# Performance work log

Hardware: AMD Instinct MI355X
Metric: run time of the kernel (lower is better)

The kernel has to match this reference:

```python
import jax, jax.numpy as jnp
import numpy as np

ALPHA = 0.2  # LeakyReLU negative slope
N, IN_DIM, OUT_DIM = 8192, 128, 64


def setup_inputs() -> dict:
    key = jax.random.key(0)
    k1, k2, k3, k4 = jax.random.split(key, 4)
    x = jax.random.normal(k1, (N, IN_DIM), dtype=jnp.float32)
    adj = jax.random.randint(k2, (N, N), 0, 2, dtype=jnp.int32)
    W = jax.random.normal(k3, (IN_DIM, OUT_DIM), dtype=jnp.float32) * 0.1
    a = jax.random.normal(k4, (2 * OUT_DIM, 1), dtype=jnp.float32) * 0.1
    return {"x": x, "adj": adj, "W": W, "a": a}


def reference(x, adj, W, a):
    # h = x @ W : [N, out]
    h = x @ W
    # e_ij = LeakyReLU(a^T [h_i || h_j]) computed as broadcast sum of the
    # two halves of the attention vector (avoids materializing [N,N,2*out]).
    a_src = a[:OUT_DIM, 0]   # [out]
    a_dst = a[OUT_DIM:, 0]   # [out]
    e = (h @ a_src)[:, None] + (h @ a_dst)[None, :]      # [N, N]
    e = jnp.where(e > 0, e, ALPHA * e)                    # LeakyReLU
    # mask non-edges, row-softmax
    e = jnp.where(adj > 0, e, jnp.float32(-9e15))
    attn = jax.nn.softmax(e, axis=-1)                     # [N, N]
    out = attn @ h                                        # [N, out]
    # concat=True -> ELU nonlinearity
    return jax.nn.elu(out)
```

## Files before the change

kernel.cpp:

```cpp
#include <hip/hip_runtime.h>
#include <hip/hip_bf16.h>
#include <cstdint>
#include <cstddef>

#define N_NODES 8192
#define IN_DIM  128
#define OUT_DIM 64
#define LRELU_ALPHA 0.2f
#define LOG2E 1.44269504f
#define NSTEP 32

using f32x16 = __attribute__((ext_vector_type(16))) float;
using bf16x8 = __attribute__((ext_vector_type(8))) short;

typedef const __attribute__((address_space(1))) int* gas_ptr;
typedef __attribute__((address_space(3))) int* las_ptr;

static __device__ __forceinline__ unsigned short f2bf(float x) {
    union { float f; unsigned u; } v; v.f = x;
    unsigned r = v.u + 0x7FFFu + ((v.u >> 16) & 1u);
    return (unsigned short)(r >> 16);
}

__global__ __launch_bounds__(256) void gat_prep(
    const float* __restrict__ x, const float* __restrict__ W,
    const float* __restrict__ a,
    float* __restrict__ svec, float* __restrict__ dvec,
    unsigned short* __restrict__ hpack)
{
    __shared__ float shA[4][8][64];
    const int tid = threadIdx.x;
    const int w   = tid >> 6;
    const int f   = tid & 63;
    const int i0  = blockIdx.x * 8;

    float acc[8];
#pragma unroll
    for (int r = 0; r < 8; ++r) acc[r] = 0.f;

    const int k0 = w * 32;
#pragma unroll 2
    for (int k = k0; k < k0 + 32; k += 4) {
        const float w0 = W[(k + 0) * OUT_DIM + f];
        const float w1 = W[(k + 1) * OUT_DIM + f];
        const float w2 = W[(k + 2) * OUT_DIM + f];
        const float w3 = W[(k + 3) * OUT_DIM + f];
#pragma unroll
        for (int r = 0; r < 8; ++r) {
            const float4 xv = *reinterpret_cast<const float4*>(
                x + (size_t)(i0 + r) * IN_DIM + k);
            acc[r] = fmaf(xv.x, w0, acc[r]);
            acc[r] = fmaf(xv.y, w1, acc[r]);
            acc[r] = fmaf(xv.z, w2, acc[r]);
            acc[r] = fmaf(xv.w, w3, acc[r]);
        }
    }
#pragma unroll
    for (int r = 0; r < 8; ++r) shA[w][r][f] = acc[r];
    __syncthreads();

    if (w == 0) {
        union { unsigned short us[8]; int4 v; } pk;
#pragma unroll
        for (int r = 0; r < 8; ++r) {
            const float hv = shA[0][r][f] + shA[1][r][f] + shA[2][r][f] + shA[3][r][f];
            pk.us[r] = f2bf(hv);
        }
        const int jb    = i0 >> 4;
        const int jhalf = (i0 >> 3) & 1;
        const int fb    = f >> 5;
        const int lidx  = (f & 31) + 32 * jhalf;
        *reinterpret_cast<int4*>(hpack + ((size_t)(jb * 2 + fb) * 64 + lidx) * 8) = pk.v;
    } else if (w == 1) {
        const float asrc = a[f];
#pragma unroll
        for (int r = 0; r < 8; ++r) {
            const float hv = shA[0][r][f] + shA[1][r][f] + shA[2][r][f] + shA[3][r][f];
            float sv = hv * asrc;
#pragma unroll
            for (int off = 32; off >= 1; off >>= 1) sv += __shfl_xor(sv, off);
            if (f == 0) svec[i0 + r] = sv * LOG2E;
        }
    } else if (w == 2) {
        const float adst = a[OUT_DIM + f];
#pragma unroll
        for (int r = 0; r < 8; ++r) {
            const float hv = shA[0][r][f] + shA[1][r][f] + shA[2][r][f] + shA[3][r][f];
            float dv = hv * adst;
#pragma unroll
            for (int off = 32; off >= 1; off >>= 1) dv += __shfl_xor(dv, off);
            if (f == 0) dvec[i0 + r] = dv * LOG2E;
        }
    }
}

__global__ __launch_bounds__(512, 2) void gat_main(
    const int* __restrict__ adj,
    const float* __restrict__ svec, const float* __restrict__ dvec,
    const unsigned short* __restrict__ hpack,
    float* __restrict__ out)
{
    union SH {
        int tiles[2][32 * 256];
        struct { float red[8][32][64]; float redden[8][32]; } r;
    };
    __shared__ SH sh;

    const int tid = threadIdx.x;
    const int w   = tid >> 6;
    const int l   = tid & 63;
    const int rb  = blockIdx.x;
    const int row = l & 31;
    const int kh  = l >> 5;
    const int i0  = rb * 32;

    const float s_i = svec[i0 + row];
    asm volatile("" :: "v"(s_i));
    const bf16x8* hp = reinterpret_cast<const bf16x8*>(hpack);

    auto stage = [&](int buf, int ss) {
        const int jt0 = ss * 256;
#pragma unroll
        for (int q = 0; q < 4; ++q) {
            const int r0 = w * 4 + q;
            const int cg = l ^ (r0 & 7);
            const int* gsrc = adj + (size_t)(i0 + r0) * N_NODES + jt0 + cg * 4;
            int* ldst = &sh.tiles[buf][r0 * 256];
            __builtin_amdgcn_global_load_lds((gas_ptr)gsrc, (las_ptr)ldst, 16, 0, 0);
        }
    };

    f32x16 acc0, acc1;
#pragma unroll
    for (int r = 0; r < 16; ++r) { acc0[r] = 0.f; acc1[r] = 0.f; }
    float den = 0.f;

    stage(0, 0);
    stage(1, 1);

    const int swz = row & 7;
    for (int s = 0; s < NSTEP; ++s) {
        const int buf = s & 1;
        const int jg  = s * 256 + w * 32;
        const int jb  = jg >> 4;

        const bf16x8 b00 = hp[(jb * 2 + 0) * 64 + l];
        const bf16x8 b01 = hp[(jb * 2 + 1) * 64 + l];
        const bf16x8 b10 = hp[(jb * 2 + 2) * 64 + l];
        const bf16x8 b11 = hp[(jb * 2 + 3) * 64 + l];
        const int j0 = jg + kh * 8;
        const float4 dA0 = *reinterpret_cast<const float4*>(dvec + j0);
        const float4 dA1 = *reinterpret_cast<const float4*>(dvec + j0 + 4);
        const float4 dB0 = *reinterpret_cast<const float4*>(dvec + j0 + 16);
        const float4 dB1 = *reinterpret_cast<const float4*>(dvec + j0 + 20);

        if (s == NSTEP - 1) asm volatile("s_waitcnt vmcnt(8)"  ::: "memory");
        else                asm volatile("s_waitcnt vmcnt(12)" ::: "memory");
        __builtin_amdgcn_s_barrier();

        const int* tb = &sh.tiles[buf][0];
        const int c00 = w * 8 + kh * 2;
        const int c10 = w * 8 + 4 + kh * 2;
        const int4 A00 = *reinterpret_cast<const int4*>(&tb[row * 256 + ((c00    ) ^ swz) * 4]);
        const int4 A01 = *reinterpret_cast<const int4*>(&tb[row * 256 + ((c00 + 1) ^ swz) * 4]);
        const int4 A10 = *reinterpret_cast<const int4*>(&tb[row * 256 + ((c10    ) ^ swz) * 4]);
        const int4 A11 = *reinterpret_cast<const int4*>(&tb[row * 256 + ((c10 + 1) ^ swz) * 4]);
        asm volatile("s_waitcnt lgkmcnt(0)" ::: "memory");
        __builtin_amdgcn_s_barrier();

        if (s + 2 < NSTEP) stage(buf, s + 2);

        const float dd0[8] = {dA0.x, dA0.y, dA0.z, dA0.w, dA1.x, dA1.y, dA1.z, dA1.w};
        const int   ia0[8] = {A00.x, A00.y, A00.z, A00.w, A01.x, A01.y, A01.z, A01.w};
        const float dd1[8] = {dB0.x, dB0.y, dB0.z, dB0.w, dB1.x, dB1.y, dB1.z, dB1.w};
        const int   ia1[8] = {A10.x, A10.y, A10.z, A10.w, A11.x, A11.y, A11.z, A11.w};

        bf16x8 af0, af1;
#pragma unroll
        for (int e = 0; e < 8; ++e) {
            float ev = s_i + dd0[e];
            ev = fmaxf(ev, LRELU_ALPHA * ev);
            float pv = __builtin_amdgcn_exp2f(ev);
            pv = (ia0[e] > 0) ? pv : 0.f;
            union { float f; unsigned u; } pu; pu.f = pv;
            pu.u &= 0xFFFF0000u;
            den += pu.f;
            af0[e] = (short)(pu.u >> 16);
        }
#pragma unroll
        for (int e = 0; e < 8; ++e) {
            float ev = s_i + dd1[e];
            ev = fmaxf(ev, LRELU_ALPHA * ev);
            float pv = __builtin_amdgcn_exp2f(ev);
            pv = (ia1[e] > 0) ? pv : 0.f;
            union { float f; unsigned u; } pu; pu.f = pv;
            pu.u &= 0xFFFF0000u;
            den += pu.f;
            af1[e] = (short)(pu.u >> 16);
        }
        acc0 = __builtin_amdgcn_mfma_f32_32x32x16_bf16(af0, b00, acc0, 0, 0, 0);
        acc1 = __builtin_amdgcn_mfma_f32_32x32x16_bf16(af0, b01, acc1, 0, 0, 0);
        acc0 = __builtin_amdgcn_mfma_f32_32x32x16_bf16(af1, b10, acc0, 0, 0, 0);
        acc1 = __builtin_amdgcn_mfma_f32_32x32x16_bf16(af1, b11, acc1, 0, 0, 0);
    }

    __syncthreads();

#pragma unroll
    for (int r = 0; r < 16; ++r) {
        const int orow = (r & 3) + 8 * (r >> 2) + 4 * kh;
        sh.r.red[w][orow][row]      = acc0[r];
        sh.r.red[w][orow][32 + row] = acc1[r];
    }
    const float dtot = den + __shfl_xor(den, 32);
    if (l < 32) sh.r.redden[w][l] = dtot;
    __syncthreads();

    for (int e = tid; e < 32 * 64; e += 512) {
        const int orow = e >> 6;
        float v = 0.f, dsum = 0.f;
#pragma unroll
        for (int ww = 0; ww < 8; ++ww) {
            v    += sh.r.red[ww][orow][e & 63];
            dsum += sh.r.redden[ww][orow];
        }
        const float o = v / dsum;
        out[(size_t)(i0 + orow) * OUT_DIM + (e & 63)] = (o > 0.f) ? o : expm1f(o);
    }
}

extern "C" void kernel_launch(void* const* d_in, const int* in_sizes, int n_in,
                              void* d_out, int out_size, void* d_ws, size_t ws_size,
                              hipStream_t stream)
{
    const float* x   = (const float*)d_in[0];
    const int*   adj = (const int*)d_in[1];
    const float* W   = (const float*)d_in[2];
    const float* a   = (const float*)d_in[3];
    float* out = (float*)d_out;

    float* svec = (float*)d_ws;
    float* dvec = svec + N_NODES;
    unsigned short* hpack = (unsigned short*)(dvec + N_NODES);

    gat_prep<<<N_NODES / 8, 256, 0, stream>>>(x, W, a, svec, dvec, hpack);
    gat_main<<<256, 512, 0, stream>>>(adj, svec, dvec, hpack, out);
}
```

Before: 73.47 us.

## Warp-specialize: producer warps bit-pack adjacency, consumer warps run softmax-MFMA

Splits the 8 waves into 4 producer waves that load adjacency rows with plain global loads and compress them into 64-bit ballot masks in LDS, and 4 consumer waves that read the bitmasks and do the exp/mask/MFMA work. Granules of 2048 columns are double-buffered so compression of the next granule overlaps compute on the current one. This replaces the direct global-to-LDS int tile staging and shrinks the LDS footprint, but halves the number of waves doing the compute and MFMA work.

Result: slower. 83.43 us (+13.6%).

```diff
diff --git a/kernel.cpp b/kernel.cpp
--- a/kernel.cpp
+++ b/kernel.cpp
@@ -8,13 +8,11 @@
 #define OUT_DIM 64
 #define LRELU_ALPHA 0.2f
 #define LOG2E 1.44269504f
-#define NSTEP 32
+#define NG 4
 
 using f32x16 = __attribute__((ext_vector_type(16))) float;
 using bf16x8 = __attribute__((ext_vector_type(8))) short;
-
-typedef const __attribute__((address_space(1))) int* gas_ptr;
-typedef __attribute__((address_space(3))) int* las_ptr;
+typedef unsigned long long u64;
 
 static __device__ __forceinline__ unsigned short f2bf(float x) {
     union { float f; unsigned u; } v; v.f = x;
@@ -101,8 +99,8 @@
     float* __restrict__ out)
 {
     union SH {
-        int tiles[2][32 * 256];
-        struct { float red[8][32][64]; float redden[8][32]; } r;
+        u64 bits[2][32][32];
+        struct { float red[4][32][64]; float redden[4][32]; } r;
     };
     __shared__ SH sh;
 
@@ -114,19 +112,37 @@
     const int kh  = l >> 5;
     const int i0  = rb * 32;
 
-    const float s_i = svec[i0 + row];
-    asm volatile("" :: "v"(s_i));
     const bf16x8* hp = reinterpret_cast<const bf16x8*>(hpack);
-
-    auto stage = [&](int buf, int ss) {
-        const int jt0 = ss * 256;
-#pragma unroll
-        for (int q = 0; q < 4; ++q) {
-            const int r0 = w * 4 + q;
-            const int cg = l ^ (r0 & 7);
-            const int* gsrc = adj + (size_t)(i0 + r0) * N_NODES + jt0 + cg * 4;
-            int* ldst = &sh.tiles[buf][r0 * 256];
-            __builtin_amdgcn_global_load_lds((gas_ptr)gsrc, (las_ptr)ldst, 16, 0, 0);
+    const float s_i = (w >= 4) ? svec[i0 + row] : 0.f;
+
+    auto loadRow = [&](int (&av)[32], int r32, int j0) {
+        const int* base = adj + (size_t)(i0 + r32) * N_NODES + j0;
+#pragma unroll
+        for (int q = 0; q < 32; ++q) av[q] = base[q * 64 + l];
+    };
+    auto packRow = [&](const int (&av)[32], int r32, int buf) {
+        unsigned lo = 0, hi = 0;
+#pragma unroll
+        for (int q = 0; q < 32; ++q) {
+            const u64 b = __ballot(av[q] != 0);
+            if (l == q) { lo = (unsigned)b; hi = (unsigned)(b >> 32); }
+        }
+        if (l < 32) sh.bits[buf][r32][l ^ (r32 & 15)] = ((u64)hi << 32) | lo;
+    };
+    auto compressGranule = [&](int g, int buf) {
+        const int j0 = g * 2048;
+        int avA[32], avB[32];
+        loadRow(avA, w * 8, j0);
+#pragma unroll
+        for (int r8 = 0; r8 < 8; ++r8) {
+            const int r32 = w * 8 + r8;
+            if (r8 & 1) {
+                if (r8 + 1 < 8) loadRow(avA, r32 + 1, j0);
+                packRow(avB, r32, buf);
+            } else {
+                if (r8 + 1 < 8) loadRow(avB, r32 + 1, j0);
+                packRow(avA, r32, buf);
+            }
         }
     };
 
@@ -135,92 +151,96 @@
     for (int r = 0; r < 16; ++r) { acc0[r] = 0.f; acc1[r] = 0.f; }
     float den = 0.f;
 
-    stage(0, 0);
-    stage(1, 1);
-
-    const int swz = row & 7;
-    for (int s = 0; s < NSTEP; ++s) {
-        const int buf = s & 1;
-        const int jg  = s * 256 + w * 32;
-        const int jb  = jg >> 4;
-
-        const bf16x8 b00 = hp[(jb * 2 + 0) * 64 + l];
-        const bf16x8 b01 = hp[(jb * 2 + 1) * 64 + l];
-        const bf16x8 b10 = hp[(jb * 2 + 2) * 64 + l];
-        const bf16x8 b11 = hp[(jb * 2 + 3) * 64 + l];
-        const int j0 = jg + kh * 8;
-        const float4 dA0 = *reinterpret_cast<const float4*>(dvec + j0);
-        const float4 dA1 = *reinterpret_cast<const float4*>(dvec + j0 + 4);
-        const float4 dB0 = *reinterpret_cast<const float4*>(dvec + j0 + 16);
-        const float4 dB1 = *reinterpret_cast<const float4*>(dvec + j0 + 20);
-
-        if (s == NSTEP - 1) asm volatile("s_waitcnt vmcnt(8)"  ::: "memory");
-        else                asm volatile("s_waitcnt vmcnt(12)" ::: "memory");
-        __builtin_amdgcn_s_barrier();
-
-        const int* tb = &sh.tiles[buf][0];
-        const int c00 = w * 8 + kh * 2;
-        const int c10 = w * 8 + 4 + kh * 2;
-        const int4 A00 = *reinterpret_cast<const int4*>(&tb[row * 256 + ((c00    ) ^ swz) * 4]);
-        const int4 A01 = *reinterpret_cast<const int4*>(&tb[row * 256 + ((c00 + 1) ^ swz) * 4]);
-        const int4 A10 = *reinterpret_cast<const int4*>(&tb[row * 256 + ((c10    ) ^ swz) * 4]);
-        const int4 A11 = *reinterpret_cast<const int4*>(&tb[row * 256 + ((c10 + 1) ^ swz) * 4]);
-        asm volatile("s_waitcnt lgkmcnt(0)" ::: "memory");
-        __builtin_amdgcn_s_barrier();
-
-        if (s + 2 < NSTEP) stage(buf, s + 2);
-
-        const float dd0[8] = {dA0.x, dA0.y, dA0.z, dA0.w, dA1.x, dA1.y, dA1.z, dA1.w};
-        const int   ia0[8] = {A00.x, A00.y, A00.z, A00.w, A01.x, A01.y, A01.z, A01.w};
-        const float dd1[8] = {dB0.x, dB0.y, dB0.z, dB0.w, dB1.x, dB1.y, dB1.z, dB1.w};
-        const int   ia1[8] = {A10.x, A10.y, A10.z, A10.w, A11.x, A11.y, A11.z, A11.w};
-
-        bf16x8 af0, af1;
-#pragma unroll
-        for (int e = 0; e < 8; ++e) {
-            float ev = s_i + dd0[e];
-            ev = fmaxf(ev, LRELU_ALPHA * ev);
-            float pv = __builtin_amdgcn_exp2f(ev);
-            pv = (ia0[e] > 0) ? pv : 0.f;
-            union { float f; unsigned u; } pu; pu.f = pv;
-            pu.u &= 0xFFFF0000u;
-            den += pu.f;
-            af0[e] = (short)(pu.u >> 16);
-        }
-#pragma unroll
-        for (int e = 0; e < 8; ++e) {
-            float ev = s_i + dd1[e];
-            ev = fmaxf(ev, LRELU_ALPHA * ev);
-            float pv = __builtin_amdgcn_exp2f(ev);
-            pv = (ia1[e] > 0) ? pv : 0.f;
-            union { float f; unsigned u; } pu; pu.f = pv;
-            pu.u &= 0xFFFF0000u;
-            den += pu.f;
-            af1[e] = (short)(pu.u >> 16);
-        }
-        acc0 = __builtin_amdgcn_mfma_f32_32x32x16_bf16(af0, b00, acc0, 0, 0, 0);
-        acc1 = __builtin_amdgcn_mfma_f32_32x32x16_bf16(af0, b01, acc1, 0, 0, 0);
-        acc0 = __builtin_amdgcn_mfma_f32_32x32x16_bf16(af1, b10, acc0, 0, 0, 0);
-        acc1 = __builtin_amdgcn_mfma_f32_32x32x16_bf16(af1, b11, acc1, 0, 0, 0);
-    }
-
+    auto computeGranule = [&](int g, int buf) {
+        const int cw = w - 4;
+#pragma unroll
+        for (int c = 0; c < 8; ++c) {
+            const int wd  = cw * 8 + c;
+            const u64 wv  = sh.bits[buf][row][wd ^ (row & 15)];
+            const int jg0 = g * 2048 + wd * 64;
+#pragma unroll
+            for (int ti = 0; ti < 2; ++ti) {
+                const int jg = jg0 + ti * 32;
+                const int jb = jg >> 4;
+                const bf16x8 b00 = hp[(jb * 2 + 0) * 64 + l];
+                const bf16x8 b01 = hp[(jb * 2 + 1) * 64 + l];
+                const bf16x8 b10 = hp[(jb * 2 + 2) * 64 + l];
+                const bf16x8 b11 = hp[(jb * 2 + 3) * 64 + l];
+                const int j0 = jg + kh * 8;
+                const float4 dA0 = *reinterpret_cast<const float4*>(dvec + j0);
+                const float4 dA1 = *reinterpret_cast<const float4*>(dvec + j0 + 4);
+                const float4 dB0 = *reinterpret_cast<const float4*>(dvec + j0 + 16);
+                const float4 dB1 = *reinterpret_cast<const float4*>(dvec + j0 + 20);
+
+                const unsigned b32 = ti ? (unsigned)(wv >> 32) : (unsigned)wv;
+                const unsigned mq0 = b32 >> (kh * 8);
+                const unsigned mq1 = b32 >> (16 + kh * 8);
+
+                const float dd0[8] = {dA0.x, dA0.y, dA0.z, dA0.w, dA1.x, dA1.y, dA1.z, dA1.w};
+                const float dd1[8] = {dB0.x, dB0.y, dB0.z, dB0.w, dB1.x, dB1.y, dB1.z, dB1.w};
+
+                bf16x8 af0, af1;
+#pragma unroll
+                for (int e = 0; e < 8; ++e) {
+                    float ev = s_i + dd0[e];
+                    ev = fmaxf(ev, LRELU_ALPHA * ev);
+                    float pv = __builtin_amdgcn_exp2f(ev);
+                    pv = ((mq0 >> e) & 1u) ? pv : 0.f;
+                    union { float f; unsigned u; } pu; pu.f = pv;
+                    pu.u &= 0xFFFF0000u;
+                    den += pu.f;
+                    af0[e] = (short)(pu.u >> 16);
+                }
+#pragma unroll
+                for (int e = 0; e < 8; ++e) {
+                    float ev = s_i + dd1[e];
+                    ev = fmaxf(ev, LRELU_ALPHA * ev);
+                    float pv = __builtin_amdgcn_exp2f(ev);
+                    pv = ((mq1 >> e) & 1u) ? pv : 0.f;
+                    union { float f; unsigned u; } pu; pu.f = pv;
+                    pu.u &= 0xFFFF0000u;
+                    den += pu.f;
+                    af1[e] = (short)(pu.u >> 16);
+                }
+                acc0 = __builtin_amdgcn_mfma_f32_32x32x16_bf16(af0, b00, acc0, 0, 0, 0);
+                acc1 = __builtin_amdgcn_mfma_f32_32x32x16_bf16(af0, b01, acc1, 0, 0, 0);
+                acc0 = __builtin_amdgcn_mfma_f32_32x32x16_bf16(af1, b10, acc0, 0, 0, 0);
+                acc1 = __builtin_amdgcn_mfma_f32_32x32x16_bf16(af1, b11, acc1, 0, 0, 0);
+            }
+        }
+    };
+
+    if (w < 4) compressGranule(0, 0);
     __syncthreads();
 
-#pragma unroll
-    for (int r = 0; r < 16; ++r) {
-        const int orow = (r & 3) + 8 * (r >> 2) + 4 * kh;
-        sh.r.red[w][orow][row]      = acc0[r];
-        sh.r.red[w][orow][32 + row] = acc1[r];
-    }
-    const float dtot = den + __shfl_xor(den, 32);
-    if (l < 32) sh.r.redden[w][l] = dtot;
+#pragma unroll 1
+    for (int g = 0; g < NG; ++g) {
+        if (w < 4) {
+            if (g + 1 < NG) compressGranule(g + 1, (g + 1) & 1);
+        } else {
+            computeGranule(g, g & 1);
+        }
+        __syncthreads();
+    }
+
+    if (w >= 4) {
+        const int cw = w - 4;
+#pragma unroll
+        for (int r = 0; r < 16; ++r) {
+            const int orow = (r & 3) + 8 * (r >> 2) + 4 * kh;
+            sh.r.red[cw][orow][row]      = acc0[r];
+            sh.r.red[cw][orow][32 + row] = acc1[r];
+        }
+        const float dtot = den + __shfl_xor(den, 32);
+        if (l < 32) sh.r.redden[cw][l] = dtot;
+    }
     __syncthreads();
 
     for (int e = tid; e < 32 * 64; e += 512) {
         const int orow = e >> 6;
         float v = 0.f, dsum = 0.f;
 #pragma unroll
-        for (int ww = 0; ww < 8; ++ww) {
+        for (int ww = 0; ww < 4; ++ww) {
             v    += sh.r.red[ww][orow][e & 63];
             dsum += sh.r.redden[ww][orow];
         }
```
